# Kernel optimization log

Hardware: AMD Instinct MI355X
Metric: run time of the kernel (lower is better)

## Reference

```python
import jax, jax.numpy as jnp
import numpy as np

DT = 0.1
T_END = 1.0
# matches python `int(t[-1] // dt)` in etd_integration
N_STEPS = int(T_END // DT)


def _expm(X, order=10, squarings=4):
    """Scaling-and-squaring Taylor matrix exponential (fixed order, jit-safe,
    differentiable). Accurate here because ||X|| is kept small by construction."""
    n = X.shape[0]
    I = jnp.eye(n, dtype=X.dtype)
    Xs = X / (2.0 ** squarings)
    term, acc = I, I
    for k in range(1, order + 1):
        term = (term @ Xs) / k
        acc = acc + term
    for _ in range(squarings):
        acc = acc @ acc
    return acc


def etd1_bch2(A, B, dt):
    """ETD1 propagators for dX/dt = A X + X B + N:
    m1_L = e^{dt A}, m1_R = e^{dt B}, m2 = A^{-1}(e^{dt A} - I) (phi1 weight)."""
    m1_L = _expm(dt * A)
    m1_R = _expm(dt * B)
    m2 = jnp.linalg.solve(A, m1_L - jnp.eye(A.shape[0], dtype=A.dtype))
    return m1_L, m1_R, m2


def reference(x, x0, adj, alpha_train, w, d):
    n = adj.shape[0]
    alph = jax.nn.sigmoid(alpha_train)[:, None]          # [n,1]
    d_c = jnp.clip(d, 0.0, 1.0)                          # [2h]
    w_mat = (w * d_c) @ w.T                              # [2h,2h]
    A = alph * 0.5 * adj - alph * 0.5 * jnp.eye(n, dtype=adj.dtype)   # [n,n]
    B = w_mat - jnp.eye(w_mat.shape[0], dtype=w_mat.dtype)            # [2h,2h]
    m1_L, m1_R, m2 = etd1_bch2(A, B, DT)
    forcing = m2 @ x0                                     # constant per step

    def step(IC, _):
        return m1_L @ IC @ m1_R + forcing, None

    z, _ = jax.lax.scan(step, x, None, length=N_STEPS)
    return z


def setup_inputs() -> dict:
    key = jax.random.key(0)
    ks = jax.random.split(key, 6)
    n, dfeat = 2048, 1024
    x = jax.random.normal(ks[0], (n, dfeat), dtype=jnp.float32)
    x0 = jax.random.normal(ks[1], (n, dfeat), dtype=jnp.float32)
    # normalized-adjacency stand-in: uniform entries scaled by 1/n (row sums ~0.5)
    adj = jax.random.uniform(ks[2], (n, n), dtype=jnp.float32) / n
    alpha_train = jax.random.normal(ks[3], (n,), dtype=jnp.float32)
    # original inits w = eye(2h); perturb slightly so math is nontrivial but e^{dtB} stays tame
    w = jnp.eye(dfeat, dtype=jnp.float32) + 0.02 * jax.random.normal(ks[4], (dfeat, dfeat), dtype=jnp.float32)
    d = jax.random.uniform(ks[5], (dfeat,), dtype=jnp.float32)
    return {"x": x, "x0": x0, "adj": adj, "alpha_train": alpha_train, "w": w, "d": d}
```

## Files before the change

kernel.cpp:

```cpp
#include <hip/hip_runtime.h>

typedef __attribute__((ext_vector_type(8))) short short8v;
typedef __attribute__((ext_vector_type(4))) float f32x4;

typedef const __attribute__((address_space(1))) void gvoid_t;
typedef __attribute__((address_space(3))) void svoid_t;

__device__ __forceinline__ unsigned short f2b(float f) {
    unsigned u = __float_as_uint(f);
    unsigned r = (u + 0x7fffu + ((u >> 16) & 1u)) >> 16;
    return (unsigned short)r;
}
__device__ __forceinline__ float b2f(unsigned short h) {
    return __uint_as_float((unsigned)h << 16);
}


__global__ void k_build_AT(const float* __restrict__ adj,
                           const float* __restrict__ alpha,
                           unsigned short* __restrict__ XAb,
                           unsigned short* __restrict__ XATb,
                           int n, float scale)
{
    __shared__ float tile[32][33];
    int bx = blockIdx.x * 32, by = blockIdx.y * 32;
    int tx = threadIdx.x, ty = threadIdx.y;
    #pragma unroll
    for (int r = 0; r < 32; r += 8) {
        int i = by + ty + r, j = bx + tx;
        float s = 1.f / (1.f + expf(-alpha[i]));
        float v = scale * s * (adj[(size_t)i * n + j] - (i == j ? 1.f : 0.f));
        XAb[(size_t)i * n + j] = f2b(v);
        tile[ty + r][tx] = v;
    }
    __syncthreads();
    #pragma unroll
    for (int r = 0; r < 32; r += 8)
        XATb[(size_t)(bx + ty + r) * n + by + tx] = f2b(tile[tx][ty + r]);
}

__global__ void k_build_EW(const float* __restrict__ w,
                           const float* __restrict__ d,
                           unsigned short* __restrict__ Eb,
                           unsigned short* __restrict__ Edb,
                           float* __restrict__ Edf, int h)
{
    int j = blockIdx.x * 256 + threadIdx.x;
    int i = blockIdx.y;
    if (j >= h) return;
    size_t idx = (size_t)i * h + j;
    float e = w[idx] - (i == j ? 1.f : 0.f);
    float dc = fminf(fmaxf(d[j], 0.f), 1.f);
    Eb[idx] = f2b(e);
    float ed = e * dc;
    Edb[idx] = f2b(ed);
    Edf[idx] = ed;
}

__global__ void k_build_R(const float* __restrict__ Ed,
                          const float* __restrict__ d,
                          float* __restrict__ R, int h, float dt)
{
    __shared__ float tile[32][33];
    int bx = blockIdx.x * 32, by = blockIdx.y * 32;
    int tx = threadIdx.x, ty = threadIdx.y;
    #pragma unroll
    for (int r = 0; r < 32; r += 8)
        tile[ty + r][tx] = Ed[(size_t)(bx + ty + r) * h + by + tx];
    __syncthreads();
    #pragma unroll
    for (int r = 0; r < 32; r += 8) {
        int i = by + ty + r, j = bx + tx;
        float v = Ed[(size_t)i * h + j] + tile[tx][ty + r];
        if (i == j) v += fminf(fmaxf(d[i], 0.f), 1.f) - 1.f;
        R[(size_t)i * h + j] = dt * v;
    }
}

__global__ void k_tsplit2(const float* __restrict__ in0,
                          const float* __restrict__ in1,
                          unsigned short* __restrict__ out0,
                          unsigned short* __restrict__ out1, int R, int C)
{
    __shared__ float tile[32][33];
    int bx = blockIdx.x * 32, by = blockIdx.y * 32;
    int tx = threadIdx.x, ty = threadIdx.y;
    #pragma unroll
    for (int r = 0; r < 32; r += 8)
        tile[ty + r][tx] = in0[(size_t)(by + ty + r) * C + bx + tx];
    __syncthreads();
    #pragma unroll
    for (int r = 0; r < 32; r += 8)
        out0[(size_t)(bx + ty + r) * R + by + tx] = f2b(tile[tx][ty + r]);
    __syncthreads();
    #pragma unroll
    for (int r = 0; r < 32; r += 8)
        tile[ty + r][tx] = in1[(size_t)(by + ty + r) * C + bx + tx];
    __syncthreads();
    #pragma unroll
    for (int r = 0; r < 32; r += 8)
        out1[(size_t)(bx + ty + r) * R + by + tx] = f2b(tile[tx][ty + r]);
}


template<int FM, int FN, int MW>
__global__ __launch_bounds__(256, MW)
void gemm_bf16(const unsigned short* __restrict__ A,
               const unsigned short* __restrict__ BT,
               float* __restrict__ C,
               float* __restrict__ C2,
               unsigned short* __restrict__ Cb,
               unsigned short* __restrict__ Cb2,
               unsigned short* __restrict__ Cb3,
               unsigned short* __restrict__ CbT,
               const float* __restrict__ D,
               const float* __restrict__ D2,
               const unsigned short* __restrict__ Db,
               int M, int N, int K,
               float alpha, float beta, float g2, float g3,
               float pa, float pb, float pc,
               float qa, float qb, float qc)
{
    constexpr int BM = FM * 32, BN = FN * 32, BK = 64;
    constexpr int AIT = BM * BK / (8 * 256);
    constexpr int BIT = BN * BK / (8 * 256);
    constexpr int LPT = AIT + BIT;
    __shared__ unsigned short As[2][BM * BK];
    __shared__ unsigned short Bs[2][BN * BK];

    int bid = blockIdx.y * gridDim.x + blockIdx.x;
    int rpx = gridDim.y >> 3;
    int q = bid & 7, c = bid >> 3;
    int by = q * rpx + (c % rpx);
    int bx = c / rpx;

    const int tid  = threadIdx.x;
    const int lane = tid & 63;
    const int wave = tid >> 6;
    const int wr = wave >> 1, wc = wave & 1;
    const int l16 = lane & 15, l4 = lane >> 4;
    const int brow = by * BM, bcol = bx * BN;

    f32x4 acc[FM][FN];
    #pragma unroll
    for (int m = 0; m < FM; ++m)
        #pragma unroll
        for (int j = 0; j < FN; ++j)
            acc[m][j] = (f32x4){0.f, 0.f, 0.f, 0.f};

    const unsigned short* Ab = A + (size_t)brow * K;
    const unsigned short* Bb = BT + (size_t)bcol * K;
    const int nt = K / BK;

    auto stage = [&](int b, int k0) {
        #pragma unroll
        for (int it = 0; it < AIT; ++it) {
            int cb = it * 256 + wave * 64;
            int ch = cb + lane;
            int r = ch >> 3, cc = ch & 7;
            int cs = cc ^ (r & 7);
            __builtin_amdgcn_global_load_lds(
                (gvoid_t*)(Ab + (size_t)r * K + k0 + cs * 8),
                (svoid_t*)(&As[b][cb * 8]), 16, 0, 0);
        }
        #pragma unroll
        for (int it = 0; it < BIT; ++it) {
            int cb = it * 256 + wave * 64;
            int ch = cb + lane;
            int r = ch >> 3, cc = ch & 7;
            int cs = cc ^ (r & 7);
            __builtin_amdgcn_global_load_lds(
                (gvoid_t*)(Bb + (size_t)r * K + k0 + cs * 8),
                (svoid_t*)(&Bs[b][cb * 8]), 16, 0, 0);
        }
    };

    stage(0, 0);
    stage(1, BK);

    for (int t = 0; t < nt; ++t) {
        const int cur = t & 1;
        if (t + 1 < nt) {
            asm volatile("s_waitcnt vmcnt(%0)" :: "i"(LPT) : "memory");
        } else {
            asm volatile("s_waitcnt vmcnt(0)" ::: "memory");
        }
        __builtin_amdgcn_s_barrier();
        asm volatile("" ::: "memory");
        __builtin_amdgcn_sched_barrier(0);

        short8v af[FM][2], bf[FN][2];
        #pragma unroll
        for (int m = 0; m < FM; ++m) {
            int r = wr * FM * 16 + m * 16 + l16;
            #pragma unroll
            for (int hf = 0; hf < 2; ++hf) {
                int cs = (hf * 4 + l4) ^ (r & 7);
                af[m][hf] = *(const short8v*)&As[cur][r * BK + cs * 8];
            }
        }
        #pragma unroll
        for (int j = 0; j < FN; ++j) {
            int r = wc * FN * 16 + j * 16 + l16;
            #pragma unroll
            for (int hf = 0; hf < 2; ++hf) {
                int cs = (hf * 4 + l4) ^ (r & 7);
                bf[j][hf] = *(const short8v*)&Bs[cur][r * BK + cs * 8];
            }
        }
        __builtin_amdgcn_s_setprio(1);
        #pragma unroll
        for (int hf = 0; hf < 2; ++hf)
            #pragma unroll
            for (int m = 0; m < FM; ++m)
                #pragma unroll
                for (int j = 0; j < FN; ++j)
                    acc[m][j] = __builtin_amdgcn_mfma_f32_16x16x32_bf16(
                        af[m][hf], bf[j][hf], acc[m][j], 0, 0, 0);
        __builtin_amdgcn_s_setprio(0);
        __builtin_amdgcn_sched_barrier(0);
        __builtin_amdgcn_s_barrier();
        asm volatile("" ::: "memory");
        if (t + 2 < nt) stage(cur, (t + 2) * BK);
    }

    #pragma unroll
    for (int m = 0; m < FM; ++m) {
        #pragma unroll
        for (int j = 0; j < FN; ++j) {
            const int row0 = brow + wr * FM * 16 + m * 16 + l4 * 4;
            const int col  = bcol + wc * FN * 16 + j * 16 + l16;
            float vv[4];
            #pragma unroll
            for (int q2 = 0; q2 < 4; ++q2) {
                size_t idx = (size_t)(row0 + q2) * N + col;
                float a0 = acc[m][j][q2];
                float v = alpha * a0;
                float dv = 0.f, dbv = 0.f;
                if (D)  { dv = D[idx]; v = fmaf(beta, dv, v); }
                if (D2) v = fmaf(g2, D2[idx], v);
                if (Db) { dbv = b2f(Db[idx]); v = fmaf(g3, dbv, v); }
                vv[q2] = v;
                if (C)  C[idx] = v;
                if (Cb) Cb[idx] = f2b(v);
                if (C2 || Cb2) {
                    float v2 = pa * a0;
                    if (D)  v2 = fmaf(pb, dv, v2);
                    if (Db) v2 = fmaf(pc, dbv, v2);
                    if (C2)  C2[idx] = v2;
                    if (Cb2) Cb2[idx] = f2b(v2);
                }
                if (Cb3) {
                    float v3 = qa * a0;
                    if (D)  v3 = fmaf(qb, dv, v3);
                    if (Db) v3 = fmaf(qc, dbv, v3);
                    Cb3[idx] = f2b(v3);
                }
            }
            if (CbT) {
                ushort4 t4;
                t4.x = f2b(vv[0]); t4.y = f2b(vv[1]);
                t4.z = f2b(vv[2]); t4.w = f2b(vv[3]);
                *reinterpret_cast<ushort4*>(&CbT[(size_t)col * M + row0]) = t4;
            }
        }
    }
}


extern "C" void kernel_launch(void* const* d_in, const int* in_sizes, int n_in,
                              void* d_out, int out_size, void* d_ws, size_t ws_size,
                              hipStream_t stream)
{
    const float* x     = (const float*)d_in[0];
    const float* x0    = (const float*)d_in[1];
    const float* adj   = (const float*)d_in[2];
    const float* alpha = (const float*)d_in[3];
    const float* w     = (const float*)d_in[4];
    const float* dvec  = (const float*)d_in[5];

    const int n = in_sizes[3];
    const int h = in_sizes[5];
    const size_t MB = 1u << 20;
    char* ws = (char*)d_ws;

    typedef unsigned short u16;
    u16*   XAb   = (u16*)(ws + 0 * MB);
    u16*   XATb  = (u16*)(ws + 8 * MB);
    u16*   Mah   = (u16*)(ws + 16 * MB);
    u16*   Pmb   = (u16*)(ws + 24 * MB);
    u16*   M3ah  = (u16*)(ws + 32 * MB);
    u16*   MbT   = (u16*)(ws + 40 * MB);
    u16*   M3bTb = (u16*)(ws + 42 * MB);
    u16*   Eb_   = (u16*)(ws + 0 * MB);
    u16*   Edb   = (u16*)(ws + 2 * MB);
    float* Edf   = (float*)(ws + 4 * MB);
    float* R     = (float*)(ws + 8 * MB);
    float* XBf   = (float*)(ws + 12 * MB);
    u16*   XBb   = (u16*)(ws + 44 * MB);
    u16*   XBT   = (u16*)(ws + 46 * MB);
    float* P2f   = (float*)(ws + 48 * MB);
    u16*   P2b   = (u16*)(ws + 52 * MB);
    float* P3f   = (float*)(ws + 54 * MB);
    u16*   P3b   = (u16*)(ws + 58 * MB);
    u16*   x0T   = (u16*)(ws + 0 * MB);
    float* Ff    = (float*)(ws + 4 * MB);
    u16*   Fb    = (u16*)(ws + 12 * MB);
    u16*   FTb   = (u16*)(ws + 44 * MB);
    u16*   ub    = (u16*)(ws + 48 * MB);
    u16*   F2b   = (u16*)(ws + 52 * MB);
    u16*   F2Tb  = (u16*)(ws + 56 * MB);
    u16*   vb    = (u16*)(ws + 60 * MB);
    float* F3f   = (float*)(ws + 64 * MB);
    u16*   zt    = (u16*)(ws + 72 * MB);
    u16*   tb16  = (u16*)(ws + 76 * MB);
    float* za    = (float*)(ws + 80 * MB);

    const dim3 blk(256);
    const dim3 gNN(n / 64, n / 64);
    const dim3 gHN(h / 32, n / 64);
    const dim3 gHH(h / 64, h / 32);
    const float dt = 0.1f;
    const u16* nu16 = nullptr;
    const float* nf32 = nullptr;

    k_build_AT<<<dim3(n / 32, n / 32), dim3(32, 8), 0, stream>>>(
        adj, alpha, XAb, XATb, n, 0.5f * dt);
    gemm_bf16<2, 2, 4><<<gNN, blk, 0, stream>>>(
        XAb, XATb, nullptr, nullptr, Mah, Pmb, M3ah, nullptr, nf32, nf32, XAb,
        n, n, n, 0.5f, 0.f, 0.f, 1.f,
        1.f / 6.f, 0.f, 0.5f, 4.5f, 0.f, 3.f);

    k_build_EW<<<dim3(h / 256, h), blk, 0, stream>>>(w, dvec, Eb_, Edb, Edf, h);
    k_build_R<<<dim3(h / 32, h / 32), dim3(32, 8), 0, stream>>>(Edf, dvec, R, h, dt);
    gemm_bf16<1, 2, 4><<<gHH, blk, 0, stream>>>(
        Edb, Eb_, XBf, nullptr, XBb, nullptr, nullptr, XBT, R, nf32, nu16,
        h, h, h, dt, 1.f, 0.f, 0.f, 0.f, 0.f, 0.f, 0.f, 0.f, 0.f);
    gemm_bf16<1, 2, 4><<<gHH, blk, 0, stream>>>(
        XBb, XBT, P2f, nullptr, P2b, nullptr, nullptr, nullptr, nf32, nf32, nu16,
        h, h, h, 1.f, 0.f, 0.f, 0.f, 0.f, 0.f, 0.f, 0.f, 0.f, 0.f);
    gemm_bf16<1, 2, 4><<<gHH, blk, 0, stream>>>(
        P2b, XBT, nullptr, P3f, nullptr, P3b, nullptr, MbT, XBf, P2f, nu16,
        h, h, h, 1.f / 6.f, 1.f, 0.5f, 0.f, 1.f, 0.f, 0.f, 0.f, 0.f, 0.f);
    gemm_bf16<1, 2, 4><<<gHH, blk, 0, stream>>>(
        P3b, XBT, nullptr, nullptr, nullptr, nullptr, nullptr, M3bTb,
        P3f, P2f, XBb,
        h, h, h, 3.375f, 4.5f, 4.5f, 3.f, 0.f, 0.f, 0.f, 0.f, 0.f, 0.f);

    k_tsplit2<<<dim3(h / 32, n / 32), dim3(32, 8), 0, stream>>>(
        x0, x, x0T, zt, n, h);

    gemm_bf16<2, 1, 4><<<gHN, blk, 0, stream>>>(
        Pmb, x0T, Ff, nullptr, Fb, nullptr, nullptr, FTb, x0, nf32, nu16,
        n, h, n, dt, dt, 0.f, 0.f, 0.f, 0.f, 0.f, 0.f, 0.f, 0.f);
    gemm_bf16<2, 1, 4><<<gHN, blk, 0, stream>>>(
        Mah, FTb, nullptr, nullptr, ub, nullptr, nullptr, nullptr, nf32, nf32, Fb,
        n, h, n, 1.f, 0.f, 0.f, 1.f, 0.f, 0.f, 0.f, 0.f, 0.f, 0.f);
    gemm_bf16<2, 1, 4><<<gHN, blk, 0, stream>>>(
        ub, MbT, nullptr, nullptr, F2b, nullptr, nullptr, F2Tb, nf32, Ff, ub,
        n, h, h, 1.f, 0.f, 1.f, 1.f, 0.f, 0.f, 0.f, 0.f, 0.f, 0.f);
    gemm_bf16<2, 1, 4><<<gHN, blk, 0, stream>>>(
        Mah, F2Tb, nullptr, nullptr, vb, nullptr, nullptr, nullptr, nf32, nf32, F2b,
        n, h, n, 1.f, 0.f, 0.f, 1.f, 0.f, 0.f, 0.f, 0.f, 0.f, 0.f);
    gemm_bf16<2, 1, 4><<<gHN, blk, 0, stream>>>(
        vb, MbT, F3f, nullptr, nullptr, nullptr, nullptr, nullptr, nf32, Ff, vb,
        n, h, h, 1.f, 0.f, 1.f, 1.f, 0.f, 0.f, 0.f, 0.f, 0.f, 0.f);

    const float* zf = x;
    for (int s = 0; s < 3; ++s) {
        gemm_bf16<2, 1, 4><<<gHN, blk, 0, stream>>>(
            M3ah, zt, nullptr, nullptr, tb16, nullptr, nullptr, nullptr,
            zf, nf32, nu16,
            n, h, n, 1.f, 1.f, 0.f, 0.f, 0.f, 0.f, 0.f, 0.f, 0.f, 0.f);
        float* zout = (s == 2) ? (float*)d_out : za;
        gemm_bf16<2, 1, 4><<<gHN, blk, 0, stream>>>(
            tb16, M3bTb, zout, nullptr, nullptr, nullptr, nullptr,
            (s == 2) ? nullptr : zt, nf32, F3f, tb16,
            n, h, h, 1.f, 0.f, 1.f, 1.f, 0.f, 0.f, 0.f, 0.f, 0.f, 0.f);
        zf = za;
    }
}
```

Baseline: 323.2 us.

## Co-launch independent GEMMs in merged grids to cut launches and fill the GPU

Replaces the per-GEMM launches with a kernel that takes two argument structs and splits its 1D grid between two independent GEMMs. The small h×h chain that builds the right propagator is interleaved with the large n-sized GEMMs, and the first z-step GEMM is co-scheduled with another one. Workspace buffers are relocated so the co-running GEMMs do not alias. This is meant to remove launch gaps and tail underutilisation from the small GEMMs, at the cost of passing struct arguments and selecting them at runtime per block.

```diff
diff --git a/kernel.cpp b/kernel.cpp
--- a/kernel.cpp
+++ b/kernel.cpp
@@ -103,23 +103,19 @@
 }
 
 
+struct GArgs {
+    const unsigned short *A, *BT;
+    float *C, *C2;
+    unsigned short *Cb, *Cb2, *Cb3, *CbT;
+    const float *D, *D2;
+    const unsigned short *Db;
+    int M, N, K, ngx, ngy;
+    float alpha, beta, g2, g3, pa, pb, pc, qa, qb, qc;
+};
+
 template<int FM, int FN, int MW>
 __global__ __launch_bounds__(256, MW)
-void gemm_bf16(const unsigned short* __restrict__ A,
-               const unsigned short* __restrict__ BT,
-               float* __restrict__ C,
-               float* __restrict__ C2,
-               unsigned short* __restrict__ Cb,
-               unsigned short* __restrict__ Cb2,
-               unsigned short* __restrict__ Cb3,
-               unsigned short* __restrict__ CbT,
-               const float* __restrict__ D,
-               const float* __restrict__ D2,
-               const unsigned short* __restrict__ Db,
-               int M, int N, int K,
-               float alpha, float beta, float g2, float g3,
-               float pa, float pb, float pc,
-               float qa, float qb, float qc)
+void gemm2(GArgs a0, GArgs a1, int nb0)
 {
     constexpr int BM = FM * 32, BN = FN * 32, BK = 64;
     constexpr int AIT = BM * BK / (8 * 256);
@@ -128,8 +124,11 @@
     __shared__ unsigned short As[2][BM * BK];
     __shared__ unsigned short Bs[2][BN * BK];
 
-    int bid = blockIdx.y * gridDim.x + blockIdx.x;
-    int rpx = gridDim.y >> 3;
+    const bool second = ((int)blockIdx.x >= nb0);
+    const GArgs& a = second ? a1 : a0;
+    int bid = (int)blockIdx.x - (second ? nb0 : 0);
+
+    int rpx = a.ngy >> 3;
     int q = bid & 7, c = bid >> 3;
     int by = q * rpx + (c % rpx);
     int bx = c / rpx;
@@ -140,6 +139,7 @@
     const int wr = wave >> 1, wc = wave & 1;
     const int l16 = lane & 15, l4 = lane >> 4;
     const int brow = by * BM, bcol = bx * BN;
+    const int K = a.K, N = a.N, M = a.M;
 
     f32x4 acc[FM][FN];
     #pragma unroll
@@ -148,8 +148,8 @@
         for (int j = 0; j < FN; ++j)
             acc[m][j] = (f32x4){0.f, 0.f, 0.f, 0.f};
 
-    const unsigned short* Ab = A + (size_t)brow * K;
-    const unsigned short* Bb = BT + (size_t)bcol * K;
+    const unsigned short* Ab = a.A + (size_t)brow * K;
+    const unsigned short* Bb = a.BT + (size_t)bcol * K;
     const int nt = K / BK;
 
     auto stage = [&](int b, int k0) {
@@ -234,39 +234,59 @@
             #pragma unroll
             for (int q2 = 0; q2 < 4; ++q2) {
                 size_t idx = (size_t)(row0 + q2) * N + col;
-                float a0 = acc[m][j][q2];
-                float v = alpha * a0;
+                float a0v = acc[m][j][q2];
+                float v = a.alpha * a0v;
                 float dv = 0.f, dbv = 0.f;
-                if (D)  { dv = D[idx]; v = fmaf(beta, dv, v); }
-                if (D2) v = fmaf(g2, D2[idx], v);
-                if (Db) { dbv = b2f(Db[idx]); v = fmaf(g3, dbv, v); }
+                if (a.D)  { dv = a.D[idx]; v = fmaf(a.beta, dv, v); }
+                if (a.D2) v = fmaf(a.g2, a.D2[idx], v);
+                if (a.Db) { dbv = b2f(a.Db[idx]); v = fmaf(a.g3, dbv, v); }
                 vv[q2] = v;
-                if (C)  C[idx] = v;
-                if (Cb) Cb[idx] = f2b(v);
-                if (C2 || Cb2) {
-                    float v2 = pa * a0;
-                    if (D)  v2 = fmaf(pb, dv, v2);
-                    if (Db) v2 = fmaf(pc, dbv, v2);
-                    if (C2)  C2[idx] = v2;
-                    if (Cb2) Cb2[idx] = f2b(v2);
+                if (a.C)  a.C[idx] = v;
+                if (a.Cb) a.Cb[idx] = f2b(v);
+                if (a.C2 || a.Cb2) {
+                    float v2 = a.pa * a0v;
+                    if (a.D)  v2 = fmaf(a.pb, dv, v2);
+                    if (a.Db) v2 = fmaf(a.pc, dbv, v2);
+                    if (a.C2)  a.C2[idx] = v2;
+                    if (a.Cb2) a.Cb2[idx] = f2b(v2);
                 }
-                if (Cb3) {
-                    float v3 = qa * a0;
-                    if (D)  v3 = fmaf(qb, dv, v3);
-                    if (Db) v3 = fmaf(qc, dbv, v3);
-                    Cb3[idx] = f2b(v3);
+                if (a.Cb3) {
+                    float v3 = a.qa * a0v;
+                    if (a.D)  v3 = fmaf(a.qb, dv, v3);
+                    if (a.Db) v3 = fmaf(a.qc, dbv, v3);
+                    a.Cb3[idx] = f2b(v3);
                 }
             }
-            if (CbT) {
+            if (a.CbT) {
                 ushort4 t4;
                 t4.x = f2b(vv[0]); t4.y = f2b(vv[1]);
                 t4.z = f2b(vv[2]); t4.w = f2b(vv[3]);
-                *reinterpret_cast<ushort4*>(&CbT[(size_t)col * M + row0]) = t4;
+                *reinterpret_cast<ushort4*>(&a.CbT[(size_t)col * M + row0]) = t4;
             }
         }
     }
 }
 
+
+typedef unsigned short u16;
+
+static GArgs mk(const u16* A, const u16* BT, float* C, float* C2,
+                u16* Cb, u16* Cb2, u16* Cb3, u16* CbT,
+                const float* D, const float* D2, const u16* Db,
+                int M, int N, int K, int ngx, int ngy,
+                float alpha, float beta, float g2, float g3,
+                float pa, float pb, float pc,
+                float qa, float qb, float qc)
+{
+    GArgs a;
+    a.A = A; a.BT = BT; a.C = C; a.C2 = C2;
+    a.Cb = Cb; a.Cb2 = Cb2; a.Cb3 = Cb3; a.CbT = CbT;
+    a.D = D; a.D2 = D2; a.Db = Db;
+    a.M = M; a.N = N; a.K = K; a.ngx = ngx; a.ngy = ngy;
+    a.alpha = alpha; a.beta = beta; a.g2 = g2; a.g3 = g3;
+    a.pa = pa; a.pb = pb; a.pc = pc; a.qa = qa; a.qb = qb; a.qc = qc;
+    return a;
+}
 
 extern "C" void kernel_launch(void* const* d_in, const int* in_sizes, int n_in,
                               void* d_out, int out_size, void* d_ws, size_t ws_size,
@@ -284,7 +304,6 @@
     const size_t MB = 1u << 20;
     char* ws = (char*)d_ws;
 
-    typedef unsigned short u16;
     u16*   XAb   = (u16*)(ws + 0 * MB);
     u16*   XATb  = (u16*)(ws + 8 * MB);
     u16*   Mah   = (u16*)(ws + 16 * MB);
@@ -292,91 +311,111 @@
     u16*   M3ah  = (u16*)(ws + 32 * MB);
     u16*   MbT   = (u16*)(ws + 40 * MB);
     u16*   M3bTb = (u16*)(ws + 42 * MB);
-    u16*   Eb_   = (u16*)(ws + 0 * MB);
-    u16*   Edb   = (u16*)(ws + 2 * MB);
-    float* Edf   = (float*)(ws + 4 * MB);
-    float* R     = (float*)(ws + 8 * MB);
-    float* XBf   = (float*)(ws + 12 * MB);
-    u16*   XBb   = (u16*)(ws + 44 * MB);
-    u16*   XBT   = (u16*)(ws + 46 * MB);
-    float* P2f   = (float*)(ws + 48 * MB);
-    u16*   P2b   = (u16*)(ws + 52 * MB);
-    float* P3f   = (float*)(ws + 54 * MB);
-    u16*   P3b   = (u16*)(ws + 58 * MB);
-    u16*   x0T   = (u16*)(ws + 0 * MB);
-    float* Ff    = (float*)(ws + 4 * MB);
-    u16*   Fb    = (u16*)(ws + 12 * MB);
-    u16*   FTb   = (u16*)(ws + 44 * MB);
-    u16*   ub    = (u16*)(ws + 48 * MB);
-    u16*   F2b   = (u16*)(ws + 52 * MB);
-    u16*   F2Tb  = (u16*)(ws + 56 * MB);
-    u16*   vb    = (u16*)(ws + 60 * MB);
-    float* F3f   = (float*)(ws + 64 * MB);
-    u16*   zt    = (u16*)(ws + 72 * MB);
-    u16*   tb16  = (u16*)(ws + 76 * MB);
-    float* za    = (float*)(ws + 80 * MB);
+    u16*   Eb_   = (u16*)(ws + 44 * MB);
+    u16*   Edb   = (u16*)(ws + 46 * MB);
+    float* Edf   = (float*)(ws + 48 * MB);
+    float* R     = (float*)(ws + 52 * MB);
+    float* XBf   = (float*)(ws + 56 * MB);
+    u16*   XBb   = (u16*)(ws + 60 * MB);
+    u16*   XBT   = (u16*)(ws + 62 * MB);
+    float* P2f   = (float*)(ws + 64 * MB);
+    u16*   P2b   = (u16*)(ws + 68 * MB);
+    float* P3f   = (float*)(ws + 70 * MB);
+    u16*   P3b   = (u16*)(ws + 74 * MB);
+    u16*   x0T   = (u16*)(ws + 76 * MB);
+    float* Ff    = (float*)(ws + 80 * MB);
+    u16*   Fb    = (u16*)(ws + 88 * MB);
+    u16*   FTb   = (u16*)(ws + 92 * MB);
+    u16*   ub    = (u16*)(ws + 96 * MB);
+    u16*   F2b   = (u16*)(ws + 100 * MB);
+    u16*   F2Tb  = (u16*)(ws + 104 * MB);
+    u16*   vb    = (u16*)(ws + 108 * MB);
+    float* F3f   = (float*)(ws + 112 * MB);
+    u16*   zt    = (u16*)(ws + 120 * MB);
+    u16*   tb16  = (u16*)(ws + 124 * MB);
+    float* za    = (float*)(ws + 128 * MB);
 
     const dim3 blk(256);
-    const dim3 gNN(n / 64, n / 64);
-    const dim3 gHN(h / 32, n / 64);
-    const dim3 gHH(h / 64, h / 32);
     const float dt = 0.1f;
-    const u16* nu16 = nullptr;
-    const float* nf32 = nullptr;
+    const u16* nu = nullptr;
+    const float* nf = nullptr;
 
     k_build_AT<<<dim3(n / 32, n / 32), dim3(32, 8), 0, stream>>>(
         adj, alpha, XAb, XATb, n, 0.5f * dt);
-    gemm_bf16<2, 2, 4><<<gNN, blk, 0, stream>>>(
-        XAb, XATb, nullptr, nullptr, Mah, Pmb, M3ah, nullptr, nf32, nf32, XAb,
-        n, n, n, 0.5f, 0.f, 0.f, 1.f,
-        1.f / 6.f, 0.f, 0.5f, 4.5f, 0.f, 3.f);
-
     k_build_EW<<<dim3(h / 256, h), blk, 0, stream>>>(w, dvec, Eb_, Edb, Edf, h);
     k_build_R<<<dim3(h / 32, h / 32), dim3(32, 8), 0, stream>>>(Edf, dvec, R, h, dt);
-    gemm_bf16<1, 2, 4><<<gHH, blk, 0, stream>>>(
-        Edb, Eb_, XBf, nullptr, XBb, nullptr, nullptr, XBT, R, nf32, nu16,
-        h, h, h, dt, 1.f, 0.f, 0.f, 0.f, 0.f, 0.f, 0.f, 0.f, 0.f);
-    gemm_bf16<1, 2, 4><<<gHH, blk, 0, stream>>>(
-        XBb, XBT, P2f, nullptr, P2b, nullptr, nullptr, nullptr, nf32, nf32, nu16,
-        h, h, h, 1.f, 0.f, 0.f, 0.f, 0.f, 0.f, 0.f, 0.f, 0.f, 0.f);
-    gemm_bf16<1, 2, 4><<<gHH, blk, 0, stream>>>(
-        P2b, XBT, nullptr, P3f, nullptr, P3b, nullptr, MbT, XBf, P2f, nu16,
-        h, h, h, 1.f / 6.f, 1.f, 0.5f, 0.f, 1.f, 0.f, 0.f, 0.f, 0.f, 0.f);
-    gemm_bf16<1, 2, 4><<<gHH, blk, 0, stream>>>(
-        P3b, XBT, nullptr, nullptr, nullptr, nullptr, nullptr, M3bTb,
-        P3f, P2f, XBb,
-        h, h, h, 3.375f, 4.5f, 4.5f, 3.f, 0.f, 0.f, 0.f, 0.f, 0.f, 0.f);
-
     k_tsplit2<<<dim3(h / 32, n / 32), dim3(32, 8), 0, stream>>>(
         x0, x, x0T, zt, n, h);
 
-    gemm_bf16<2, 1, 4><<<gHN, blk, 0, stream>>>(
-        Pmb, x0T, Ff, nullptr, Fb, nullptr, nullptr, FTb, x0, nf32, nu16,
-        n, h, n, dt, dt, 0.f, 0.f, 0.f, 0.f, 0.f, 0.f, 0.f, 0.f);
-    gemm_bf16<2, 1, 4><<<gHN, blk, 0, stream>>>(
-        Mah, FTb, nullptr, nullptr, ub, nullptr, nullptr, nullptr, nf32, nf32, Fb,
-        n, h, n, 1.f, 0.f, 0.f, 1.f, 0.f, 0.f, 0.f, 0.f, 0.f, 0.f);
-    gemm_bf16<2, 1, 4><<<gHN, blk, 0, stream>>>(
-        ub, MbT, nullptr, nullptr, F2b, nullptr, nullptr, F2Tb, nf32, Ff, ub,
-        n, h, h, 1.f, 0.f, 1.f, 1.f, 0.f, 0.f, 0.f, 0.f, 0.f, 0.f);
-    gemm_bf16<2, 1, 4><<<gHN, blk, 0, stream>>>(
-        Mah, F2Tb, nullptr, nullptr, vb, nullptr, nullptr, nullptr, nf32, nf32, F2b,
-        n, h, n, 1.f, 0.f, 0.f, 1.f, 0.f, 0.f, 0.f, 0.f, 0.f, 0.f);
-    gemm_bf16<2, 1, 4><<<gHN, blk, 0, stream>>>(
-        vb, MbT, F3f, nullptr, nullptr, nullptr, nullptr, nullptr, nf32, Ff, vb,
-        n, h, h, 1.f, 0.f, 1.f, 1.f, 0.f, 0.f, 0.f, 0.f, 0.f, 0.f);
-
-    const float* zf = x;
+    {
+        GArgs gA1 = mk(XAb, XATb, nullptr, nullptr, Mah, Pmb, M3ah, nullptr,
+                       nf, nf, XAb, n, n, n, n / 64, n / 64,
+                       0.5f, 0.f, 0.f, 1.f, 1.f / 6.f, 0.f, 0.5f, 4.5f, 0.f, 3.f);
+        GArgs gB1 = mk(Edb, Eb_, XBf, nullptr, XBb, nullptr, nullptr, XBT,
+                       R, nf, nu, h, h, h, h / 64, h / 64,
+                       dt, 1.f, 0.f, 0.f, 0.f, 0.f, 0.f, 0.f, 0.f, 0.f);
+        gemm2<2, 2, 4><<<dim3(1024 + 256), blk, 0, stream>>>(gA1, gB1, 1024);
+    }
+
+    {
+        GArgs gF = mk(Pmb, x0T, Ff, nullptr, Fb, nullptr, nullptr, FTb,
+                      x0, nf, nu, n, h, n, h / 32, n / 64,
+                      dt, dt, 0.f, 0.f, 0.f, 0.f, 0.f, 0.f, 0.f, 0.f);
+        GArgs gB2 = mk(XBb, XBT, P2f, nullptr, P2b, nullptr, nullptr, nullptr,
+                       nf, nf, nu, h, h, h, h / 32, h / 64,
+                       1.f, 0.f, 0.f, 0.f, 0.f, 0.f, 0.f, 0.f, 0.f, 0.f);
+        gemm2<2, 1, 4><<<dim3(1024 + 512), blk, 0, stream>>>(gF, gB2, 1024);
+    }
+
+    {
+        GArgs gU = mk(Mah, FTb, nullptr, nullptr, ub, nullptr, nullptr, nullptr,
+                      nf, nf, Fb, n, h, n, h / 32, n / 64,
+                      1.f, 0.f, 0.f, 1.f, 0.f, 0.f, 0.f, 0.f, 0.f, 0.f);
+        GArgs gB3 = mk(P2b, XBT, nullptr, P3f, nullptr, P3b, nullptr, MbT,
+                       XBf, P2f, nu, h, h, h, h / 32, h / 64,
+                       1.f / 6.f, 1.f, 0.5f, 0.f, 1.f, 0.f, 0.f, 0.f, 0.f, 0.f);
+        gemm2<2, 1, 4><<<dim3(1024 + 512), blk, 0, stream>>>(gU, gB3, 1024);
+    }
+
+    {
+        GArgs gF2 = mk(ub, MbT, nullptr, nullptr, F2b, nullptr, nullptr, F2Tb,
+                       nf, Ff, ub, n, h, h, h / 32, n / 64,
+                       1.f, 0.f, 1.f, 1.f, 0.f, 0.f, 0.f, 0.f, 0.f, 0.f);
+        GArgs gB4 = mk(P3b, XBT, nullptr, nullptr, nullptr, nullptr, nullptr, M3bTb,
+                       P3f, P2f, XBb, h, h, h, h / 32, h / 64,
+                       3.375f, 4.5f, 4.5f, 3.f, 0.f, 0.f, 0.f, 0.f, 0.f, 0.f);
+        gemm2<2, 1, 4><<<dim3(1024 + 512), blk, 0, stream>>>(gF2, gB4, 1024);
+    }
+
+    {
+        GArgs gV = mk(Mah, F2Tb, nullptr, nullptr, vb, nullptr, nullptr, nullptr,
+                      nf, nf, F2b, n, h, n, h / 32, n / 64,
+                      1.f, 0.f, 0.f, 1.f, 0.f, 0.f, 0.f, 0.f, 0.f, 0.f);
+        GArgs gG1 = mk(M3ah, zt, nullptr, nullptr, tb16, nullptr, nullptr, nullptr,
+                       x, nf, nu, n, h, n, h / 32, n / 64,
+                       1.f, 1.f, 0.f, 0.f, 0.f, 0.f, 0.f, 0.f, 0.f, 0.f);
+        gemm2<2, 1, 4><<<dim3(1024 + 1024), blk, 0, stream>>>(gV, gG1, 1024);
+    }
+
+    {
+        GArgs g = mk(vb, MbT, F3f, nullptr, nullptr, nullptr, nullptr, nullptr,
+                     nf, Ff, vb, n, h, h, h / 32, n / 64,
+                     1.f, 0.f, 1.f, 1.f, 0.f, 0.f, 0.f, 0.f, 0.f, 0.f);
+        gemm2<2, 1, 4><<<dim3(1024), blk, 0, stream>>>(g, g, 1024);
+    }
+
     for (int s = 0; s < 3; ++s) {
-        gemm_bf16<2, 1, 4><<<gHN, blk, 0, stream>>>(
-            M3ah, zt, nullptr, nullptr, tb16, nullptr, nullptr, nullptr,
-            zf, nf32, nu16,
-            n, h, n, 1.f, 1.f, 0.f, 0.f, 0.f, 0.f, 0.f, 0.f, 0.f, 0.f);
+        if (s > 0) {
+            GArgs g = mk(M3ah, zt, nullptr, nullptr, tb16, nullptr, nullptr,
+                         nullptr, za, nf, nu, n, h, n, h / 32, n / 64,
+                         1.f, 1.f, 0.f, 0.f, 0.f, 0.f, 0.f, 0.f, 0.f, 0.f);
+            gemm2<2, 1, 4><<<dim3(1024), blk, 0, stream>>>(g, g, 1024);
+        }
         float* zout = (s == 2) ? (float*)d_out : za;
-        gemm_bf16<2, 1, 4><<<gHN, blk, 0, stream>>>(
-            tb16, M3bTb, zout, nullptr, nullptr, nullptr, nullptr,
-            (s == 2) ? nullptr : zt, nf32, F3f, tb16,
-            n, h, h, 1.f, 0.f, 1.f, 1.f, 0.f, 0.f, 0.f, 0.f, 0.f, 0.f);
-        zf = za;
-    }
-}
+        GArgs g = mk(tb16, M3bTb, zout, nullptr, nullptr, nullptr, nullptr,
+                     (s == 2) ? nullptr : zt, nf, F3f, tb16,
+                     n, h, h, h / 32, n / 64,
+                     1.f, 0.f, 1.f, 1.f, 0.f, 0.f, 0.f, 0.f, 0.f, 0.f);
+        gemm2<2, 1, 4><<<dim3(1024), blk, 0, stream>>>(g, g, 1024);
+    }
+}
```

Result: faster. 296.2 us (-8.3%).
